# Kernel optimization log

Hardware: AMD Instinct MI355X
Metric: run time of the kernel (lower is better)

The kernel has to match this reference:

```python
import jax, jax.numpy as jnp
import numpy as np

B, N, P = 8, 64, 128
DNODE, DEDGE, DEMB = 2048, 1024, 512
E = B * N * N


def setup_inputs() -> dict:
    key = jax.random.key(0)
    ks = jax.random.split(key, 12)
    x = jax.random.normal(ks[0], (B, N, DNODE), dtype=jnp.float32)
    interaction_feature = jax.random.normal(ks[1], (B, N, N, DEDGE), dtype=jnp.float32)
    s = 0.02
    W_phi = jax.random.normal(ks[2], (DNODE, DEMB), dtype=jnp.float32) * s
    b_phi = jax.random.normal(ks[3], (DEMB,), dtype=jnp.float32) * s
    W_psi = jax.random.normal(ks[4], (DNODE, DEMB), dtype=jnp.float32) * s
    b_psi = jax.random.normal(ks[5], (DEMB,), dtype=jnp.float32) * s
    W_node = jax.random.normal(ks[6], (DNODE, DEMB), dtype=jnp.float32) * s
    b_node = jax.random.normal(ks[7], (DEMB,), dtype=jnp.float32) * s
    W_rel = jax.random.normal(ks[8], (DEDGE, DEMB), dtype=jnp.float32) * s
    b_rel = jax.random.normal(ks[9], (DEMB,), dtype=jnp.float32) * s
    pairs = jax.random.randint(ks[10], (B, P, 2), 0, N, dtype=jnp.int32)
    # edge_locating_tensor: rows (batch, src, dst) covering the proposed edge set
    bb, ii, jj = jnp.meshgrid(jnp.arange(B), jnp.arange(N), jnp.arange(N), indexing='ij')
    edge_locating_tensor = jnp.stack([bb.ravel(), ii.ravel(), jj.ravel()], axis=1).astype(jnp.int32)  # [E,3]
    return {"x": x, "interaction_feature": interaction_feature, "W_phi": W_phi, "b_phi": b_phi,
            "W_psi": W_psi, "b_psi": b_psi, "W_node": W_node, "b_node": b_node,
            "W_rel": W_rel, "b_rel": b_rel, "pairs": pairs, "edge_locating_tensor": edge_locating_tensor}


def _lookup_edge(elt, b_idx, i0, i1):
    # boolean-mask argmax lookup, faithful to torch argmax(loc0*loc1*loc2)
    # elt: [E,3]; b_idx,i0,i1: [B,P] -> loc: [B,P] indices into edge list
    m = (elt[None, None, :, 0] == b_idx[:, :, None]) \
        & (elt[None, None, :, 1] == i0[:, :, None]) \
        & (elt[None, None, :, 2] == i1[:, :, None])  # [B,P,E]
    return jnp.argmax(m, axis=-1)


def reference(x, interaction_feature, W_phi, b_phi, W_psi, b_psi,
              W_node, b_node, W_rel, b_rel, pairs, edge_locating_tensor):
    # relationship proposal scoring: all-pairs einsum + sigmoid
    phi = x @ W_phi + b_phi                                    # [B,N,512]
    psi = x @ W_psi + b_psi                                    # [B,N,512]
    relatedness_score = jax.nn.sigmoid(jnp.einsum('bik,bjk->bij', phi, psi))  # [B,N,N]

    # node / relationship-node embedders
    node_emb = x @ W_node + b_node                             # [B,N,512]
    elt = edge_locating_tensor
    rel_feats = interaction_feature[elt[:, 0], elt[:, 1], elt[:, 2]]  # [E,1024] gather
    edge_emb = rel_feats @ W_rel + b_rel                       # [E,512]

    # classifier input construction (gather/argmax/scatter hot path, vectorized)
    ind0, ind1 = pairs[..., 0], pairs[..., 1]                  # [B,P]
    b_idx = jnp.broadcast_to(jnp.arange(B, dtype=jnp.int32)[:, None], ind0.shape)
    emb0 = node_emb[b_idx, ind0]                               # [B,P,512]
    emb1 = node_emb[b_idx, ind1]
    first_half = (emb0 + emb1) * 0.5                           # aggregate 'mean'

    loc_fwd = _lookup_edge(elt, b_idx, ind0, ind1)             # [B,P]
    loc_rev = _lookup_edge(elt, b_idx, ind1, ind0)
    e1 = edge_emb[loc_fwd]                                     # [B,P,512]
    e2 = edge_emb[loc_rev]
    second_half = (e1 + e2) * 0.5

    classifier_input = jnp.concatenate([first_half, second_half], axis=-1)  # [B,P,1024]
    return relatedness_score, classifier_input
```

## Files before the change

kernel.cpp:

```cpp
#include <hip/hip_runtime.h>
#include <hip/hip_bf16.h>


typedef _Float16 h16;
typedef h16 h16x4 __attribute__((ext_vector_type(4)));
typedef h16 h16x8 __attribute__((ext_vector_type(8)));
typedef float f32x4 __attribute__((ext_vector_type(4)));

static const long O_W3T  = 0;
static const long O_WREL = 6291456;
static const long O_XH   = 7340032;
static const long O_G    = 9437184;
static const long O_B3   = 11534336;
static const long O_YH   = 11540480;

__global__ __launch_bounds__(256) void k_prep(
    const float* __restrict__ Wphi, const float* __restrict__ Wpsi,
    const float* __restrict__ Wnode, const float* __restrict__ Wrel,
    const float* __restrict__ x, const float* __restrict__ bphi,
    const float* __restrict__ bpsi, const float* __restrict__ bnode,
    const float* __restrict__ feat, const int* __restrict__ pairs,
    h16* __restrict__ W3t, h16* __restrict__ Wrelt, h16* __restrict__ xh,
    float* __restrict__ b3, h16* __restrict__ G) {
  __shared__ float t[32][33];
  int bid = blockIdx.x, tid = threadIdx.x;
  if (bid < 3584) {
    const float* src; h16* dst; int K, tk, tn;
    if (bid < 3072) {
      int mat = bid >> 10, rem = bid & 1023;
      tk = rem >> 4; tn = rem & 15;
      src = mat == 0 ? Wphi : (mat == 1 ? Wpsi : Wnode);
      K = 2048; dst = W3t + (long)mat * 512 * 2048;
    } else {
      int rem = bid - 3072;
      tk = rem >> 4; tn = rem & 15;
      src = Wrel; K = 1024; dst = Wrelt;
    }
    {
      int row = tid >> 3, c4 = (tid & 7) * 4;
      float4 v = *(const float4*)(src + (long)(tk*32 + row)*512 + tn*32 + c4);
      t[row][c4+0] = v.x; t[row][c4+1] = v.y; t[row][c4+2] = v.z; t[row][c4+3] = v.w;
    }
    __syncthreads();
    {
      int n = tid >> 3, k4 = (tid & 7) * 4;
      h16x4 o = { (h16)t[k4+0][n], (h16)t[k4+1][n], (h16)t[k4+2][n], (h16)t[k4+3][n] };
      *(h16x4*)(dst + (long)(tn*32 + n)*K + tk*32 + k4) = o;
    }
  } else if (bid < 4102) {
    int b2 = bid - 3584;
    if (b2 < 512) {
      int idx = (b2*256 + tid) * 8;
      const float4* xv = (const float4*)(x + idx);
      float4 v0 = xv[0], v1 = xv[1];
      h16x8 o;
      o[0]=(h16)v0.x; o[1]=(h16)v0.y; o[2]=(h16)v0.z; o[3]=(h16)v0.w;
      o[4]=(h16)v1.x; o[5]=(h16)v1.y; o[6]=(h16)v1.z; o[7]=(h16)v1.w;
      *(h16x8*)(xh + idx) = o;
    } else {
      int i = (b2 - 512)*256 + tid;
      if (i < 1536) b3[i] = i < 512 ? bphi[i] : (i < 1024 ? bpsi[i-512] : bnode[i-1024]);
    }
  } else {
    int r = bid - 4102;
    int b = r >> 7;
    int i0 = pairs[r*2], i1 = pairs[r*2+1];
    const float4* f0 = (const float4*)(feat + (long)((b*64 + i0)*64 + i1) * 1024);
    const float4* f1 = (const float4*)(feat + (long)((b*64 + i1)*64 + i0) * 1024);
    float4 a = f0[tid], c = f1[tid];
    h16x4 o;
    o[0]=(h16)(0.5f*(a.x+c.x)); o[1]=(h16)(0.5f*(a.y+c.y));
    o[2]=(h16)(0.5f*(a.z+c.z)); o[3]=(h16)(0.5f*(a.w+c.w));
    *(h16x4*)(G + (long)r*1024 + tid*4) = o;
  }
}

__device__ __forceinline__ void mfma_compute(
    const h16 (*__restrict__ As)[72], const h16 (*__restrict__ Bs)[72],
    int wm, int wn, int fr, int kg, f32x4 acc[2][2]) {
#pragma unroll
  for (int kc = 0; kc < 2; ++kc) {
    int kb = kc*32 + kg;
    h16x8 fa0 = *(const h16x8*)&As[wm*32 + fr][kb];
    h16x8 fa1 = *(const h16x8*)&As[wm*32 + 16 + fr][kb];
    h16x8 fb0 = *(const h16x8*)&Bs[wn*32 + fr][kb];
    h16x8 fb1 = *(const h16x8*)&Bs[wn*32 + 16 + fr][kb];
    acc[0][0] = __builtin_amdgcn_mfma_f32_16x16x32_f16(fa0, fb0, acc[0][0], 0,0,0);
    acc[0][1] = __builtin_amdgcn_mfma_f32_16x16x32_f16(fa0, fb1, acc[0][1], 0,0,0);
    acc[1][0] = __builtin_amdgcn_mfma_f32_16x16x32_f16(fa1, fb0, acc[1][0], 0,0,0);
    acc[1][1] = __builtin_amdgcn_mfma_f32_16x16x32_f16(fa1, fb1, acc[1][1], 0,0,0);
  }
}

__device__ __forceinline__ void mfma_compute8(
    const h16 (*__restrict__ As)[72], const h16 (*__restrict__ Bs)[72],
    int wm, int wn, int fr, int kg, f32x4 acc[2]) {
#pragma unroll
  for (int kc = 0; kc < 2; ++kc) {
    int kb = kc*32 + kg;
    h16x8 fa0 = *(const h16x8*)&As[wm*32 + fr][kb];
    h16x8 fa1 = *(const h16x8*)&As[wm*32 + 16 + fr][kb];
    h16x8 fb  = *(const h16x8*)&Bs[wn*16 + fr][kb];
    acc[0] = __builtin_amdgcn_mfma_f32_16x16x32_f16(fa0, fb, acc[0], 0,0,0);
    acc[1] = __builtin_amdgcn_mfma_f32_16x16x32_f16(fa1, fb, acc[1], 0,0,0);
  }
}

__global__ __launch_bounds__(512) void k_gemm(
    const h16* __restrict__ xh, const h16* __restrict__ W3t,
    const float* __restrict__ b3, h16* __restrict__ Yh,
    const h16* __restrict__ G, const h16* __restrict__ Wrelt,
    const float* __restrict__ brel, float* __restrict__ out) {
  __shared__ __align__(16) h16 As[2][64][72];
  __shared__ __align__(16) h16 Bs[2][64][72];
  int bid = blockIdx.x, tid = threadIdx.x;
  int lane = tid & 63, wave = tid >> 6;
  int wm = wave >> 2, wn = wave & 3;
  int srow = tid >> 3, skp = (tid & 7) * 8;
  int fr = lane & 15, kg = (lane >> 4) * 8;

  int isEdge = bid >= 192;
  int ntile = isEdge ? 2 : 1;
#pragma unroll 1
  for (int ti = 0; ti < ntile; ++ti) {
    if (ti) __syncthreads();
    const h16 *A, *Bt; int K, tileM, tileN;
    if (!isEdge) {
      A = xh; Bt = W3t; K = 2048;
      tileM = (bid / 24) * 64; tileN = (bid % 24) * 64;
    } else {
      int e = (bid - 192) * 2 + ti;
      A = G; Bt = Wrelt; K = 1024;
      tileM = (e >> 3) * 64; tileN = (e & 7) * 64;
    }
    const h16* Agp = A + (long)(tileM + srow) * K + skp;
    const h16* Bgp = Bt + (long)(tileN + srow) * K + skp;
    f32x4 acc[2] = {};
    h16x8 ra = *(const h16x8*)(Agp);
    h16x8 rb = *(const h16x8*)(Bgp);
    *(h16x8*)&As[0][srow][skp] = ra;
    *(h16x8*)&Bs[0][srow][skp] = rb;
    __syncthreads();
    int cur = 0;
#pragma unroll 1
    for (int k0 = 64; k0 < K; k0 += 64) {
      ra = *(const h16x8*)(Agp + k0);
      rb = *(const h16x8*)(Bgp + k0);
      mfma_compute8(As[cur], Bs[cur], wm, wn, fr, kg, acc);
      int nxt = cur ^ 1;
      *(h16x8*)&As[nxt][srow][skp] = ra;
      *(h16x8*)&Bs[nxt][srow][skp] = rb;
      __syncthreads();
      cur = nxt;
    }
    mfma_compute8(As[cur], Bs[cur], wm, wn, fr, kg, acc);

    int r0 = 4 * (lane >> 4);
#pragma unroll
    for (int m = 0; m < 2; ++m) {
      int row = tileM + wm*32 + m*16 + r0;
      int col = tileN + wn*16 + fr;
      if (!isEdge) {
        float bb = b3[col];
#pragma unroll
        for (int r = 0; r < 4; ++r)
          Yh[(long)(row + r) * 1536 + col] = (h16)(acc[m][r] + bb);
      } else {
        float bb = brel[col];
#pragma unroll
        for (int r = 0; r < 4; ++r)
          out[32768 + 512 + (long)(row + r) * 1024 + col] = acc[m][r] + bb;
      }
    }
  }
}

#define GEMM_PIPELINE(Agp, Bgp, K)                                        \
  {                                                                       \
    h16x8 ra0 = *(const h16x8*)(Agp);                                     \
    h16x8 ra1 = *(const h16x8*)(Agp + 8);                                 \
    h16x8 rb0 = *(const h16x8*)(Bgp);                                     \
    h16x8 rb1 = *(const h16x8*)(Bgp + 8);                                 \
    *(h16x8*)&As[0][srow][skp]   = ra0;                                   \
    *(h16x8*)&As[0][srow][skp+8] = ra1;                                   \
    *(h16x8*)&Bs[0][srow][skp]   = rb0;                                   \
    *(h16x8*)&Bs[0][srow][skp+8] = rb1;                                   \
    __syncthreads();                                                      \
    int cur = 0;                                                          \
    for (int k0 = 64; k0 < (K); k0 += 64) {                               \
      ra0 = *(const h16x8*)(Agp + k0);                                    \
      ra1 = *(const h16x8*)(Agp + k0 + 8);                                \
      rb0 = *(const h16x8*)(Bgp + k0);                                    \
      rb1 = *(const h16x8*)(Bgp + k0 + 8);                                \
      mfma_compute(As[cur], Bs[cur], wm, wn, fr, kg, acc);                \
      int nxt = cur ^ 1;                                                  \
      *(h16x8*)&As[nxt][srow][skp]   = ra0;                               \
      *(h16x8*)&As[nxt][srow][skp+8] = ra1;                               \
      *(h16x8*)&Bs[nxt][srow][skp]   = rb0;                               \
      *(h16x8*)&Bs[nxt][srow][skp+8] = rb1;                               \
      __syncthreads();                                                    \
      cur = nxt;                                                          \
    }                                                                     \
    mfma_compute(As[cur], Bs[cur], wm, wn, fr, kg, acc);                  \
  }

__global__ __launch_bounds__(256) void k_epilogue(
    const h16* __restrict__ Yh, const int* __restrict__ pairs,
    float* __restrict__ out) {
  __shared__ __align__(16) h16 As[2][64][72];
  __shared__ __align__(16) h16 Bs[2][64][72];
  int bid = blockIdx.x, tid = threadIdx.x;
  if (bid < 8) {
    int lane = tid & 63, wave = tid >> 6;
    int wm = wave >> 1, wn = wave & 1;
    int srow = tid >> 2, skp = (tid & 3) * 16;
    int fr = lane & 15, kg = (lane >> 4) * 8;
    const h16* Ab = Yh + (long)bid * 64 * 1536;
    const h16* Agp = Ab + (long)srow * 1536 + skp;
    const h16* Bgp = Ab + (long)srow * 1536 + 512 + skp;
    f32x4 acc[2][2] = {};
    GEMM_PIPELINE(Agp, Bgp, 512);
    int r0 = 4 * (lane >> 4), c0 = lane & 15;
    float* ob = out + (long)bid * 4096;
#pragma unroll
    for (int m = 0; m < 2; ++m)
#pragma unroll
      for (int n = 0; n < 2; ++n) {
        int row = wm*32 + m*16 + r0;
        int col = wn*32 + n*16 + c0;
#pragma unroll
        for (int r = 0; r < 4; ++r) {
          float s = acc[m][n][r];
          ob[(long)(row + r) * 64 + col] = 1.f / (1.f + expf(-s));
        }
      }
  } else {
    int r = bid - 8;
    int b = r >> 7;
    int i0 = pairs[r*2], i1 = pairs[r*2+1];
    const h16* n0 = Yh + (long)(b*64 + i0)*1536 + 1024;
    const h16* n1 = Yh + (long)(b*64 + i1)*1536 + 1024;
    float* o = out + 32768 + (long)r*1024;
    for (int c = tid; c < 512; c += 256)
      o[c] = 0.5f*((float)n0[c] + (float)n1[c]);
  }
}

extern "C" void kernel_launch(void* const* d_in, const int* in_sizes, int n_in,
                              void* d_out, int out_size, void* d_ws, size_t ws_size,
                              hipStream_t stream) {
  const float* x     = (const float*)d_in[0];
  const float* feat  = (const float*)d_in[1];
  const float* Wphi  = (const float*)d_in[2];
  const float* bphi  = (const float*)d_in[3];
  const float* Wpsi  = (const float*)d_in[4];
  const float* bpsi  = (const float*)d_in[5];
  const float* Wnode = (const float*)d_in[6];
  const float* bnode = (const float*)d_in[7];
  const float* Wrel  = (const float*)d_in[8];
  const float* brel  = (const float*)d_in[9];
  const int*   pairs = (const int*)d_in[10];
  float* out = (float*)d_out;
  char* ws = (char*)d_ws;

  h16*   W3t   = (h16*)(ws + O_W3T);
  h16*   Wrelt = (h16*)(ws + O_WREL);
  h16*   xh    = (h16*)(ws + O_XH);
  h16*   G     = (h16*)(ws + O_G);
  float* b3    = (float*)(ws + O_B3);
  h16*   Yh    = (h16*)(ws + O_YH);

  k_prep<<<dim3(5126), dim3(256), 0, stream>>>(
      Wphi, Wpsi, Wnode, Wrel, x, bphi, bpsi, bnode, feat, pairs,
      W3t, Wrelt, xh, b3, G);
  k_gemm<<<dim3(256), dim3(512), 0, stream>>>(
      xh, W3t, b3, Yh, G, Wrelt, brel, out);
  k_epilogue<<<dim3(1032), dim3(256), 0, stream>>>(Yh, pairs, out);
}
```

Measured before the change: 38.18 us.

## Use direct global-to-LDS loads with triple buffering and XOR swizzle in GEMM

Replaces the register-staged double-buffered GEMM mainloop with a triple-buffered pipeline that uses global_load_lds to copy tiles straight into LDS. An XOR swizzle replaces the padded LDS rows to avoid bank conflicts. Waits use explicit vmcnt counters plus raw barriers, and the K loop is fully unrolled through a template. The aim is to overlap global loads with MFMA work and cut VGPR traffic. The cost is hand-written synchronisation that relies on the ordering of the inline asm and its vmcnt counts.

```diff
diff --git a/kernel.cpp b/kernel.cpp
--- a/kernel.cpp
+++ b/kernel.cpp
@@ -92,18 +92,46 @@
   }
 }
 
-__device__ __forceinline__ void mfma_compute8(
-    const h16 (*__restrict__ As)[72], const h16 (*__restrict__ Bs)[72],
-    int wm, int wn, int fr, int kg, f32x4 acc[2]) {
-#pragma unroll
-  for (int kc = 0; kc < 2; ++kc) {
-    int kb = kc*32 + kg;
-    h16x8 fa0 = *(const h16x8*)&As[wm*32 + fr][kb];
-    h16x8 fa1 = *(const h16x8*)&As[wm*32 + 16 + fr][kb];
-    h16x8 fb  = *(const h16x8*)&Bs[wn*16 + fr][kb];
-    acc[0] = __builtin_amdgcn_mfma_f32_16x16x32_f16(fa0, fb, acc[0], 0,0,0);
-    acc[1] = __builtin_amdgcn_mfma_f32_16x16x32_f16(fa1, fb, acc[1], 0,0,0);
-  }
+template<int S>
+__device__ __forceinline__ void gemm_tile(
+    const h16* Ag, const h16* Bg,
+    h16 (*Ab3)[64][64], h16 (*Bb3)[64][64],
+    int w8, int baseA0, int baseA1, int baseB, int m7, int ch0,
+    f32x4 acc[2]) {
+#define STG(t_, b_) do {                                                      \
+    __builtin_amdgcn_global_load_lds(                                         \
+        (const __attribute__((address_space(1))) unsigned int*)(Ag + (t_)*64),\
+        (__attribute__((address_space(3))) unsigned int*)&Ab3[b_][w8][0],     \
+        16, 0, 0);                                                            \
+    __builtin_amdgcn_global_load_lds(                                         \
+        (const __attribute__((address_space(1))) unsigned int*)(Bg + (t_)*64),\
+        (__attribute__((address_space(3))) unsigned int*)&Bb3[b_][w8][0],     \
+        16, 0, 0); } while (0)
+
+  STG(0, 0);
+  STG(1, 1);
+  asm volatile("s_waitcnt vmcnt(2)\n\ts_barrier" ::: "memory");
+#pragma unroll
+  for (int t = 0; t < S; ++t) {
+    const int cur = t % 3, nb = (t + 2) % 3;
+    if (t + 2 < S) STG(t + 2, nb);
+    const char* Ac = (const char*)Ab3[cur];
+    const char* Bc = (const char*)Bb3[cur];
+#pragma unroll
+    for (int kc = 0; kc < 2; ++kc) {
+      int sw = ((kc*4 + ch0) ^ m7) << 4;
+      h16x8 fa0 = *(const h16x8*)(Ac + baseA0 + sw);
+      h16x8 fa1 = *(const h16x8*)(Ac + baseA1 + sw);
+      h16x8 fb  = *(const h16x8*)(Bc + baseB  + sw);
+      acc[0] = __builtin_amdgcn_mfma_f32_16x16x32_f16(fa0, fb, acc[0], 0,0,0);
+      acc[1] = __builtin_amdgcn_mfma_f32_16x16x32_f16(fa1, fb, acc[1], 0,0,0);
+    }
+    if (t + 1 < S) {
+      if (t + 2 < S) asm volatile("s_waitcnt vmcnt(2)\n\ts_barrier" ::: "memory");
+      else           asm volatile("s_waitcnt vmcnt(0)\n\ts_barrier" ::: "memory");
+    }
+  }
+#undef STG
 }
 
 __global__ __launch_bounds__(512) void k_gemm(
@@ -111,62 +139,50 @@
     const float* __restrict__ b3, h16* __restrict__ Yh,
     const h16* __restrict__ G, const h16* __restrict__ Wrelt,
     const float* __restrict__ brel, float* __restrict__ out) {
-  __shared__ __align__(16) h16 As[2][64][72];
-  __shared__ __align__(16) h16 Bs[2][64][72];
+  __shared__ __align__(16) h16 Ab3[3][64][64];
+  __shared__ __align__(16) h16 Bb3[3][64][64];
   int bid = blockIdx.x, tid = threadIdx.x;
   int lane = tid & 63, wave = tid >> 6;
   int wm = wave >> 2, wn = wave & 3;
-  int srow = tid >> 3, skp = (tid & 7) * 8;
-  int fr = lane & 15, kg = (lane >> 4) * 8;
-
-  int isEdge = bid >= 192;
-  int ntile = isEdge ? 2 : 1;
-#pragma unroll 1
-  for (int ti = 0; ti < ntile; ++ti) {
-    if (ti) __syncthreads();
-    const h16 *A, *Bt; int K, tileM, tileN;
-    if (!isEdge) {
-      A = xh; Bt = W3t; K = 2048;
-      tileM = (bid / 24) * 64; tileN = (bid % 24) * 64;
-    } else {
-      int e = (bid - 192) * 2 + ti;
-      A = G; Bt = Wrelt; K = 1024;
-      tileM = (e >> 3) * 64; tileN = (e & 7) * 64;
-    }
-    const h16* Agp = A + (long)(tileM + srow) * K + skp;
-    const h16* Bgp = Bt + (long)(tileN + srow) * K + skp;
+  int fr = lane & 15, ch0 = lane >> 4, m7 = fr & 7;
+  int rw = tid >> 3;
+  int cs = (tid & 7) ^ (rw & 7);
+  int w8 = wave * 8;
+  int baseA0 = (wm*32 + fr) * 128;
+  int baseA1 = (wm*32 + 16 + fr) * 128;
+  int baseB  = (wn*16 + fr) * 128;
+  int r0 = 4 * (lane >> 4);
+
+  if (bid < 192) {
+    int tileM = (bid / 24) * 64, tileN = (bid % 24) * 64;
+    const h16* Ag = xh  + (long)(tileM + rw) * 2048 + cs * 8;
+    const h16* Bg = W3t + (long)(tileN + rw) * 2048 + cs * 8;
     f32x4 acc[2] = {};
-    h16x8 ra = *(const h16x8*)(Agp);
-    h16x8 rb = *(const h16x8*)(Bgp);
-    *(h16x8*)&As[0][srow][skp] = ra;
-    *(h16x8*)&Bs[0][srow][skp] = rb;
-    __syncthreads();
-    int cur = 0;
-#pragma unroll 1
-    for (int k0 = 64; k0 < K; k0 += 64) {
-      ra = *(const h16x8*)(Agp + k0);
-      rb = *(const h16x8*)(Bgp + k0);
-      mfma_compute8(As[cur], Bs[cur], wm, wn, fr, kg, acc);
-      int nxt = cur ^ 1;
-      *(h16x8*)&As[nxt][srow][skp] = ra;
-      *(h16x8*)&Bs[nxt][srow][skp] = rb;
-      __syncthreads();
-      cur = nxt;
-    }
-    mfma_compute8(As[cur], Bs[cur], wm, wn, fr, kg, acc);
-
-    int r0 = 4 * (lane >> 4);
+    gemm_tile<32>(Ag, Bg, Ab3, Bb3, w8, baseA0, baseA1, baseB, m7, ch0, acc);
+    int col = tileN + wn*16 + fr;
+    float bb = b3[col];
 #pragma unroll
     for (int m = 0; m < 2; ++m) {
       int row = tileM + wm*32 + m*16 + r0;
+#pragma unroll
+      for (int r = 0; r < 4; ++r)
+        Yh[(long)(row + r) * 1536 + col] = (h16)(acc[m][r] + bb);
+    }
+  } else {
+#pragma unroll 1
+    for (int ti = 0; ti < 2; ++ti) {
+      if (ti) __syncthreads();
+      int e = (bid - 192) * 2 + ti;
+      int tileM = (e >> 3) * 64, tileN = (e & 7) * 64;
+      const h16* Ag = G     + (long)(tileM + rw) * 1024 + cs * 8;
+      const h16* Bg = Wrelt + (long)(tileN + rw) * 1024 + cs * 8;
+      f32x4 acc[2] = {};
+      gemm_tile<16>(Ag, Bg, Ab3, Bb3, w8, baseA0, baseA1, baseB, m7, ch0, acc);
       int col = tileN + wn*16 + fr;
-      if (!isEdge) {
-        float bb = b3[col];
-#pragma unroll
-        for (int r = 0; r < 4; ++r)
-          Yh[(long)(row + r) * 1536 + col] = (h16)(acc[m][r] + bb);
-      } else {
-        float bb = brel[col];
+      float bb = brel[col];
+#pragma unroll
+      for (int m = 0; m < 2; ++m) {
+        int row = tileM + wm*32 + m*16 + r0;
 #pragma unroll
         for (int r = 0; r < 4; ++r)
           out[32768 + 512 + (long)(row + r) * 1024 + col] = acc[m][r] + bb;
```

After: 36.40 us. 1.05x faster.
